# Performance work log

Measured on AMD Instinct MI355X. Metric: run time of the kernel, lower is better.

The kernel has to match this reference:

```python
import jax, jax.numpy as jnp
import numpy as np
from jax import lax

UP = 2
K = 3
IN_C, OUT_C = 64, 64
PAD = K // 2  # 1
WEIGHT_GAIN = 1.0 / np.sqrt(IN_C * K * K)
ACT_GAIN = np.sqrt(2.0)  # lrelu def_gain
CLAMP = 256.0
LRELU_ALPHA = 0.2


def setup_inputs() -> dict:
    key = jax.random.key(0)
    k1, k2 = jax.random.split(key)
    x = jax.random.normal(k1, (16, IN_C, 128, 128), dtype=jnp.float32)
    weight = jax.random.normal(k2, (OUT_C, IN_C, K, K), dtype=jnp.float32)
    bias = jnp.zeros((OUT_C,), dtype=jnp.float32)
    # upfirdn2d.setup_filter((1,3,3,1)): outer product, normalized to sum 1
    a = jnp.array([1.0, 3.0, 3.0, 1.0], dtype=jnp.float32)
    f = jnp.outer(a, a)
    f = f / jnp.sum(f)  # 4x4 separable FIR filter
    return {"x": x, "weight": weight, "bias": bias, "f": f}


def _upfirdn2d_up2(x, f):
    # zero-insertion upsample by 2 + pad + FIR filter, gain = up**2
    N, C, H, W = x.shape
    fw = f.shape[-1]  # 4
    # conv2d_resample padding adjustment for up>1 on top of base padding k//2
    p0 = PAD + (fw + UP - 1) // 2  # 3
    p1 = PAD + (fw - UP) // 2      # 2
    fk = jnp.tile((f * (UP * UP))[None, None], (C, 1, 1, 1))  # [C,1,4,4] depthwise
    # lhs_dilation=2 gives 2H-1 samples; add (UP-1) extra right/bottom zeros to
    # match upfirdn's 2H zero-inserted signal.
    return lax.conv_general_dilated(
        x, fk, window_strides=(1, 1),
        padding=((p0, p1 + UP - 1), (p0, p1 + UP - 1)),
        lhs_dilation=(UP, UP),
        feature_group_count=C,
        dimension_numbers=("NCHW", "OIHW", "NCHW"))


def reference(x, weight, bias, f):
    h = _upfirdn2d_up2(x, f)  # [N, C, 2H+2, 2W+2]
    # conv: flip_weight = (up == 1) = False -> true convolution (flip kernel)
    w = (weight * WEIGHT_GAIN)[:, :, ::-1, ::-1]
    y = lax.conv_general_dilated(
        h, w, window_strides=(1, 1), padding="VALID",
        dimension_numbers=("NCHW", "OIHW", "NCHW"))  # [N, OUT_C, 2H, 2W]
    # fused bias + lrelu + gain + clamp (bias_act with gain=1)
    y = y + bias[None, :, None, None]
    y = jnp.where(y >= 0, y, LRELU_ALPHA * y) * ACT_GAIN
    y = jnp.clip(y, -CLAMP, CLAMP)
    return y
```

## Files before the change

### kernel.cpp

```cpp
#include <hip/hip_runtime.h>

typedef float f32x16 __attribute__((ext_vector_type(16)));
typedef float f32x2  __attribute__((ext_vector_type(2)));
typedef short bf16x8 __attribute__((ext_vector_type(8)));

#define NB 16
#define CI 64
#define CO 64
#define Hh 128
#define Ww 128

__device__ short g_A[9 * 4 * 8 * 64 * 8];
__device__ short g_xh[(size_t)NB * Hh * Ww * CI];

__device__ inline short f2bf(float f) {
  union { float f; unsigned u; } v; v.f = f;
  unsigned r = (v.u + 0x7FFF + ((v.u >> 16) & 1)) >> 16;
  return (short)r;
}

__global__ __launch_bounds__(256) void build_filters(const float* __restrict__ w) {
  const int ef = blockIdx.x * 256 + threadIdx.x;
  if (ef >= 147456) return;
  const int e   = ef & 7;
  const int l   = (ef >> 3) & 63;
  const int mg  = (ef >> 9) & 7;
  const int ks  = (ef >> 12) & 3;
  const int tap = ef >> 14;
  const int m   = mg * 32 + (l & 31);
  const int par = m >> 6, oc = m & 63;
  const int ic  = ks * 16 + (l >> 5) * 8 + e;
  const int py = par >> 1, px = par & 1;
  const int dyi = tap / 3, dxi = tap % 3;
  const int my = 2 * dyi + 1 - py;
  const int mx = 2 * dxi + 1 - px;
  const float FF[4] = {0.25f, 0.75f, 0.75f, 0.25f};
  const float* wp = w + (oc * CI + ic) * 9;
  float s = 0.f;
  #pragma unroll
  for (int ky = 0; ky < 3; ++ky) {
    const int iy = my - ky;
    if (iy < 0 || iy > 3) continue;
    #pragma unroll
    for (int kx = 0; kx < 3; ++kx) {
      const int ix = mx - kx;
      if (ix < 0 || ix > 3) continue;
      s += wp[(2 - ky) * 3 + (2 - kx)] * (FF[iy] * FF[ix]);
    }
  }
  g_A[ef] = f2bf(s * (1.0f / 24.0f));
}

__global__ __launch_bounds__(256) void to_nhwc(const float* __restrict__ x) {
  const int b = blockIdx.x;
  const int n = b >> 7, y = b & 127;
  for (int u = threadIdx.x; u < 1024; u += 256) {
    const int xx = u >> 3, icb = u & 7;
    bf16x8 o;
    #pragma unroll
    for (int j = 0; j < 8; ++j)
      o[j] = f2bf(x[(((size_t)n * CI + icb * 8 + j) * Hh + y) * Ww + xx]);
    *(bf16x8*)(g_xh + (((size_t)n * Hh + y) * Ww + xx) * CI + icb * 8) = o;
  }
}

#define XS_BASE 65536
#define CH_STR  5200

__global__ __launch_bounds__(512, 2) void mfma_conv(const float* __restrict__ bias,
                                                    float* __restrict__ out) {
  __shared__ short lds[53568];

  const int tid = threadIdx.x;
  const int l   = tid & 63;
  const int wid = tid >> 6;
  const int wm  = wid >> 2;
  const int wn  = wid & 3;
  const int n   = blockIdx.y;
  const int ty0 = blockIdx.x >> 3, tx0 = blockIdx.x & 7;
  const int qb  = ty0 * 16, pb = tx0 * 16;

  auto stage_A = [&](int tap, int buf) {
    const char* gs = (const char*)g_A + tap * 32768 + wid * 4096 + l * 16;
    char* ls = (char*)lds + buf * 32768 + wid * 4096;
    #pragma unroll
    for (int r = 0; r < 4; ++r)
      __builtin_amdgcn_global_load_lds(
          (__attribute__((address_space(1))) void*)(gs + r * 1024),
          (__attribute__((address_space(3))) void*)(ls + r * 1024),
          16, 0, 0);
  };

  stage_A(0, 0);

  const size_t xbase = (size_t)n * (Hh * Ww * CI);
  for (int u = tid; u < 2592; u += 512) {
    const int icb8 = u & 7, pix = u >> 3;
    const int yy = pix / 18, xx = pix - yy * 18;
    const int gy = qb - 1 + yy, gx = pb - 1 + xx;
    bf16x8 v = {};
    if ((unsigned)gy < (unsigned)Hh && (unsigned)gx < (unsigned)Ww)
      v = *(const bf16x8*)(g_xh + xbase + (size_t)(gy * Ww + gx) * CI + icb8 * 8);
    *(bf16x8*)((char*)lds + XS_BASE + icb8 * CH_STR + pix * 16) = v;
  }

  f32x16 acc[4][2];
  #pragma unroll
  for (int mf = 0; mf < 4; ++mf)
    #pragma unroll
    for (int nf = 0; nf < 2; ++nf)
      #pragma unroll
      for (int r = 0; r < 16; ++r) acc[mf][nf][r] = 0.f;

  const int p    = l & 15;
  const int kg2  = l >> 5;
  const int qh   = (l >> 4) & 1;
  int bbase[2];
  #pragma unroll
  for (int nf = 0; nf < 2; ++nf)
    bbase[nf] = XS_BASE + kg2 * CH_STR + ((wn * 4 + nf * 2 + qh) * 18 + p) * 16;

  #pragma unroll
  for (int tap = 0; tap < 9; ++tap) {
    asm volatile("s_waitcnt vmcnt(0)" ::: "memory");
    __syncthreads();
    if (tap < 8) stage_A(tap + 1, (tap + 1) & 1);
    const int buf = (tap & 1) * 32768;
    const int dyi = tap / 3, dxi = tap % 3;
    const int bsh = (dyi * 18 + dxi) * 16;
    __builtin_amdgcn_s_setprio(1);
    #pragma unroll
    for (int ks = 0; ks < 4; ++ks) {
      bf16x8 a[4], b[2];
      #pragma unroll
      for (int mf = 0; mf < 4; ++mf)
        a[mf] = *(const bf16x8*)((const char*)lds + buf + ks * 8192 + (wm * 4 + mf) * 1024 + l * 16);
      #pragma unroll
      for (int nf = 0; nf < 2; ++nf)
        b[nf] = *(const bf16x8*)((const char*)lds + bbase[nf] + ks * (2 * CH_STR) + bsh);
      #pragma unroll
      for (int mf = 0; mf < 4; ++mf)
        #pragma unroll
        for (int nf = 0; nf < 2; ++nf)
          acc[mf][nf] = __builtin_amdgcn_mfma_f32_32x32x16_bf16(a[mf], b[nf], acc[mf][nf], 0, 0, 0);
    }
    __builtin_amdgcn_s_setprio(0);
  }

  float* outp = out + ((size_t)(n * CO) << 16);
  const int col = l & 31;
  const int pe  = col & 15;
  #pragma unroll
  for (int mf = 0; mf < 2; ++mf) {
    #pragma unroll
    for (int nf = 0; nf < 2; ++nf) {
      const int q = wn * 4 + nf * 2 + (col >> 4);
      const int y = 2 * (qb + q) + wm;
      const int xd = 2 * (pb + pe);
      #pragma unroll
      for (int reg = 0; reg < 16; ++reg) {
        const int row = (reg & 3) + 8 * (reg >> 2) + 4 * kg2;
        const int oc  = mf * 32 + row;
        const float bj = bias[oc];
        float v0 = acc[mf][nf][reg] + bj;
        float v1 = acc[mf + 2][nf][reg] + bj;
        v0 = (v0 >= 0.f ? v0 : 0.2f * v0) * 1.4142135623730951f;
        v1 = (v1 >= 0.f ? v1 : 0.2f * v1) * 1.4142135623730951f;
        v0 = fminf(256.f, fmaxf(-256.f, v0));
        v1 = fminf(256.f, fmaxf(-256.f, v1));
        f32x2 o; o[0] = v0; o[1] = v1;
        *(f32x2*)(outp + ((size_t)oc << 16) + y * 256 + xd) = o;
      }
    }
  }
}

extern "C" void kernel_launch(void* const* d_in, const int* in_sizes, int n_in,
                              void* d_out, int out_size, void* d_ws, size_t ws_size,
                              hipStream_t stream) {
  const float* x    = (const float*)d_in[0];
  const float* w    = (const float*)d_in[1];
  const float* bias = (const float*)d_in[2];
  float* out = (float*)d_out;

  build_filters<<<576, 256, 0, stream>>>(w);
  to_nhwc<<<2048, 256, 0, stream>>>(x);
  mfma_conv<<<dim3(64, NB), 512, 0, stream>>>(bias, out);
}
```

Baseline: 137.1 us.

## Keep filter fragments in registers, shrink conv tile, transpose input via LDS

The conv kernel now loads filter (A) fragments straight from global memory into registers, prefetching the next tap after each k-step, in place of double-buffering them in LDS. This removes the per-tap barriers. The tile shrinks to 8x16 input pixels with 256 threads and twice as many blocks, which cuts LDS use. The filter rows are reordered so each MFMA lane pair maps to adjacent output x-parities, and outputs use nontemporal stores. The NHWC conversion now stages a row through swizzled LDS so global reads are coalesced, at the cost of more register pressure and repeated global filter loads per block.

```diff
diff --git a/kernel.cpp b/kernel.cpp
--- a/kernel.cpp
+++ b/kernel.cpp
@@ -1,6 +1,7 @@
 #include <hip/hip_runtime.h>
 
 typedef float f32x16 __attribute__((ext_vector_type(16)));
+typedef float f32x4  __attribute__((ext_vector_type(4)));
 typedef float f32x2  __attribute__((ext_vector_type(2)));
 typedef short bf16x8 __attribute__((ext_vector_type(8)));
 
@@ -27,10 +28,11 @@
   const int mg  = (ef >> 9) & 7;
   const int ks  = (ef >> 12) & 3;
   const int tap = ef >> 14;
-  const int m   = mg * 32 + (l & 31);
-  const int par = m >> 6, oc = m & 63;
+  const int r   = l & 31;
+  const int px  = r & 1;
+  const int py  = mg >> 2;
+  const int oc  = (mg & 3) * 16 + (r >> 1);
   const int ic  = ks * 16 + (l >> 5) * 8 + e;
-  const int py = par >> 1, px = par & 1;
   const int dyi = tap / 3, dxi = tap % 3;
   const int my = 2 * dyi + 1 - py;
   const int mx = 2 * dxi + 1 - px;
@@ -52,57 +54,66 @@
 }
 
 __global__ __launch_bounds__(256) void to_nhwc(const float* __restrict__ x) {
+  __shared__ alignas(16) char xt[64 * 512];
   const int b = blockIdx.x;
   const int n = b >> 7, y = b & 127;
-  for (int u = threadIdx.x; u < 1024; u += 256) {
-    const int xx = u >> 3, icb = u & 7;
+  const int tid = threadIdx.x;
+  #pragma unroll
+  for (int it = 0; it < 8; ++it) {
+    const int idx = tid + it * 256;
+    const int ic = idx >> 5, xq = idx & 31;
+    const f32x4 v = *(const f32x4*)(x + (((size_t)n * CI + ic) * Hh + y) * Ww + xq * 4);
+    *(f32x4*)(xt + ic * 512 + ((xq * 16) ^ (((ic >> 3) & 7) * 16))) = v;
+  }
+  __syncthreads();
+  #pragma unroll
+  for (int it = 0; it < 4; ++it) {
+    const int idx = tid + it * 256;
+    const int icb = idx & 7, xp = idx >> 3;
     bf16x8 o;
     #pragma unroll
-    for (int j = 0; j < 8; ++j)
-      o[j] = f2bf(x[(((size_t)n * CI + icb * 8 + j) * Hh + y) * Ww + xx]);
-    *(bf16x8*)(g_xh + (((size_t)n * Hh + y) * Ww + xx) * CI + icb * 8) = o;
+    for (int j = 0; j < 8; ++j) {
+      const int ic = icb * 8 + j;
+      const float f = *(const float*)(xt + ic * 512 + (((xp >> 2) * 16) ^ (icb * 16)) + (xp & 3) * 4);
+      o[j] = f2bf(f);
+    }
+    *(bf16x8*)(g_xh + (((size_t)n * Hh + y) * Ww + xp) * CI + icb * 8) = o;
   }
 }
 
-#define XS_BASE 65536
-#define CH_STR  5200
+#define CH_STR 2896
 
-__global__ __launch_bounds__(512, 2) void mfma_conv(const float* __restrict__ bias,
+__global__ __launch_bounds__(256, 2) void mfma_conv(const float* __restrict__ bias,
                                                     float* __restrict__ out) {
-  __shared__ short lds[53568];
+  __shared__ alignas(16) char xs[8 * CH_STR];
 
   const int tid = threadIdx.x;
   const int l   = tid & 63;
   const int wid = tid >> 6;
-  const int wm  = wid >> 2;
-  const int wn  = wid & 3;
+  const int wm  = wid >> 1;
+  const int wn  = wid & 1;
   const int n   = blockIdx.y;
   const int ty0 = blockIdx.x >> 3, tx0 = blockIdx.x & 7;
-  const int qb  = ty0 * 16, pb = tx0 * 16;
+  const int qb  = ty0 * 8, pb = tx0 * 16;
 
-  auto stage_A = [&](int tap, int buf) {
-    const char* gs = (const char*)g_A + tap * 32768 + wid * 4096 + l * 16;
-    char* ls = (char*)lds + buf * 32768 + wid * 4096;
+  bf16x8 a[4][4];
+  #pragma unroll
+  for (int ks = 0; ks < 4; ++ks)
     #pragma unroll
-    for (int r = 0; r < 4; ++r)
-      __builtin_amdgcn_global_load_lds(
-          (__attribute__((address_space(1))) void*)(gs + r * 1024),
-          (__attribute__((address_space(3))) void*)(ls + r * 1024),
-          16, 0, 0);
-  };
-
-  stage_A(0, 0);
+    for (int mf = 0; mf < 4; ++mf)
+      a[ks][mf] = *(const bf16x8*)(g_A + ((ks * 8 + wm * 4 + mf) * 512) + l * 8);
 
   const size_t xbase = (size_t)n * (Hh * Ww * CI);
-  for (int u = tid; u < 2592; u += 512) {
+  for (int u = tid; u < 1440; u += 256) {
     const int icb8 = u & 7, pix = u >> 3;
     const int yy = pix / 18, xx = pix - yy * 18;
     const int gy = qb - 1 + yy, gx = pb - 1 + xx;
     bf16x8 v = {};
     if ((unsigned)gy < (unsigned)Hh && (unsigned)gx < (unsigned)Ww)
       v = *(const bf16x8*)(g_xh + xbase + (size_t)(gy * Ww + gx) * CI + icb8 * 8);
-    *(bf16x8*)((char*)lds + XS_BASE + icb8 * CH_STR + pix * 16) = v;
+    *(bf16x8*)(xs + icb8 * CH_STR + pix * 16) = v;
   }
+  __syncthreads();
 
   f32x16 acc[4][2];
   #pragma unroll
@@ -112,64 +123,58 @@
       #pragma unroll
       for (int r = 0; r < 16; ++r) acc[mf][nf][r] = 0.f;
 
-  const int p    = l & 15;
-  const int kg2  = l >> 5;
-  const int qh   = (l >> 4) & 1;
+  const int col = l & 31, kg2 = l >> 5;
+  const int p = col & 15, qh = col >> 4;
   int bbase[2];
   #pragma unroll
   for (int nf = 0; nf < 2; ++nf)
-    bbase[nf] = XS_BASE + kg2 * CH_STR + ((wn * 4 + nf * 2 + qh) * 18 + p) * 16;
+    bbase[nf] = kg2 * CH_STR + ((wn * 4 + nf * 2 + qh) * 18 + p) * 16;
 
   #pragma unroll
   for (int tap = 0; tap < 9; ++tap) {
-    asm volatile("s_waitcnt vmcnt(0)" ::: "memory");
-    __syncthreads();
-    if (tap < 8) stage_A(tap + 1, (tap + 1) & 1);
-    const int buf = (tap & 1) * 32768;
     const int dyi = tap / 3, dxi = tap % 3;
     const int bsh = (dyi * 18 + dxi) * 16;
-    __builtin_amdgcn_s_setprio(1);
     #pragma unroll
     for (int ks = 0; ks < 4; ++ks) {
-      bf16x8 a[4], b[2];
-      #pragma unroll
-      for (int mf = 0; mf < 4; ++mf)
-        a[mf] = *(const bf16x8*)((const char*)lds + buf + ks * 8192 + (wm * 4 + mf) * 1024 + l * 16);
+      bf16x8 b[2];
       #pragma unroll
       for (int nf = 0; nf < 2; ++nf)
-        b[nf] = *(const bf16x8*)((const char*)lds + bbase[nf] + ks * (2 * CH_STR) + bsh);
+        b[nf] = *(const bf16x8*)(xs + bbase[nf] + ks * (2 * CH_STR) + bsh);
+      __builtin_amdgcn_s_setprio(1);
       #pragma unroll
       for (int mf = 0; mf < 4; ++mf)
         #pragma unroll
         for (int nf = 0; nf < 2; ++nf)
-          acc[mf][nf] = __builtin_amdgcn_mfma_f32_32x32x16_bf16(a[mf], b[nf], acc[mf][nf], 0, 0, 0);
+          acc[mf][nf] = __builtin_amdgcn_mfma_f32_32x32x16_bf16(a[ks][mf], b[nf], acc[mf][nf], 0, 0, 0);
+      __builtin_amdgcn_s_setprio(0);
+      if (tap < 8) {
+        #pragma unroll
+        for (int mf = 0; mf < 4; ++mf)
+          a[ks][mf] = *(const bf16x8*)(g_A + (((tap + 1) * 4 + ks) * 8 + wm * 4 + mf) * 512 + l * 8);
+      }
     }
-    __builtin_amdgcn_s_setprio(0);
   }
 
   float* outp = out + ((size_t)(n * CO) << 16);
-  const int col = l & 31;
-  const int pe  = col & 15;
   #pragma unroll
-  for (int mf = 0; mf < 2; ++mf) {
+  for (int mf = 0; mf < 4; ++mf) {
     #pragma unroll
     for (int nf = 0; nf < 2; ++nf) {
-      const int q = wn * 4 + nf * 2 + (col >> 4);
+      const int q = wn * 4 + nf * 2 + qh;
       const int y = 2 * (qb + q) + wm;
-      const int xd = 2 * (pb + pe);
+      const int xd = 2 * (pb + p);
       #pragma unroll
-      for (int reg = 0; reg < 16; ++reg) {
-        const int row = (reg & 3) + 8 * (reg >> 2) + 4 * kg2;
-        const int oc  = mf * 32 + row;
+      for (int rp = 0; rp < 8; ++rp) {
+        const int oc = mf * 16 + (rp & 1) + 4 * (rp >> 1) + 2 * kg2;
         const float bj = bias[oc];
-        float v0 = acc[mf][nf][reg] + bj;
-        float v1 = acc[mf + 2][nf][reg] + bj;
+        float v0 = acc[mf][nf][2 * rp]     + bj;
+        float v1 = acc[mf][nf][2 * rp + 1] + bj;
         v0 = (v0 >= 0.f ? v0 : 0.2f * v0) * 1.4142135623730951f;
         v1 = (v1 >= 0.f ? v1 : 0.2f * v1) * 1.4142135623730951f;
         v0 = fminf(256.f, fmaxf(-256.f, v0));
         v1 = fminf(256.f, fmaxf(-256.f, v1));
         f32x2 o; o[0] = v0; o[1] = v1;
-        *(f32x2*)(outp + ((size_t)oc << 16) + y * 256 + xd) = o;
+        __builtin_nontemporal_store(o, (f32x2*)(outp + ((size_t)oc << 16) + y * 256 + xd));
       }
     }
   }
@@ -185,5 +190,5 @@
 
   build_filters<<<576, 256, 0, stream>>>(w);
   to_nhwc<<<2048, 256, 0, stream>>>(x);
-  mfma_conv<<<dim3(64, NB), 512, 0, stream>>>(bias, out);
+  mfma_conv<<<dim3(128, NB), 256, 0, stream>>>(bias, out);
 }
```

Result: faster. 115.5 us (-15.8%).
